# Performance work log

Measured on AMD Instinct MI355X. Metric: run time of the kernel, lower is better.

The kernel has to match this reference:

```python
import jax, jax.numpy as jnp
import numpy as np

LOSS_WEIGHT = 1.0

def setup_inputs() -> dict:
    key = jax.random.key(0)
    k1, k2 = jax.random.split(key)
    B, M, N = 4, 8192, 8192
    pred_colors = jax.random.uniform(k1, (B, M, 3), dtype=jnp.float32)
    gt_colors = jax.random.uniform(k2, (B, N, 3), dtype=jnp.float32)
    return {"pred_colors": pred_colors, "gt_colors": gt_colors}

def reference(pred_colors, gt_colors):
    # torch.cdist(p=2): Euclidean distance matrix [B, M, N]
    # ||a-b||^2 = ||a||^2 + ||b||^2 - 2 a.b
    a2 = jnp.sum(pred_colors * pred_colors, axis=-1)  # [B, M]
    b2 = jnp.sum(gt_colors * gt_colors, axis=-1)      # [B, N]
    ab = jnp.einsum('bmd,bnd->bmn', pred_colors, gt_colors)  # [B, M, N]
    d2 = a2[:, :, None] + b2[:, None, :] - 2.0 * ab
    dists = jnp.sqrt(jnp.maximum(d2, 0.0))
    min_dists = jnp.min(dists, axis=2)  # [B, M]
    return min_dists.mean() * LOSS_WEIGHT
```

## Files before the change

kernel.cpp:

```cpp
#include <hip/hip_runtime.h>
#include <math.h>


constexpr int B    = 4;
constexpr int M    = 8192;
constexpr int N    = 8192;
constexpr int BM   = B * M;
constexpr int TPB  = 256;
constexpr int RPT  = 8;
constexpr int PPB  = TPB * RPT;
constexpr int MBLK = M / PPB;
constexpr int TILE = 1024;

template <int NSEG, bool FINAL>
__global__ __launch_bounds__(TPB)
void k_min(const float* __restrict__ pred, const float* __restrict__ gt,
           float* __restrict__ ws_min, float* __restrict__ out)
{
  constexpr int S  = N / NSEG;
  constexpr int CH = (TILE < NSEG ? TILE : NSEG);
  const int bid = blockIdx.x;
  const int seg = bid % S;
  const int mb  = (bid / S) % MBLK;
  const int b   = bid / (S * MBLK);
  const int t   = threadIdx.x;

  __shared__ float4 tile[CH];

  float cx[RPT], cy[RPT], cz[RPT], mn[RPT];
  const int mbase = mb * PPB + t;
#pragma unroll
  for (int r = 0; r < RPT; ++r) {
    const float* a = pred + ((size_t)b * M + (mbase + r * TPB)) * 3;
    cx[r] = -2.0f * a[0];
    cy[r] = -2.0f * a[1];
    cz[r] = -2.0f * a[2];
    mn[r] = 3.0e38f;
  }

  const int nbase = seg * NSEG;
  for (int n0 = 0; n0 < NSEG; n0 += CH) {
    __syncthreads();
    for (int i = t; i < CH; i += TPB) {
      const float* g = gt + ((size_t)b * N + (nbase + n0 + i)) * 3;
      float gx = g[0], gy = g[1], gz = g[2];
      tile[i] = make_float4(gx, gy, gz, fmaf(gx, gx, fmaf(gy, gy, gz * gz)));
    }
    __syncthreads();
#pragma unroll 2
    for (int n = 0; n < CH; n += 2) {
      const float4 g0 = tile[n];
      const float4 g1 = tile[n + 1];
#pragma unroll
      for (int r = 0; r < RPT; ++r) {
        float s0 = fmaf(cx[r], g0.x, fmaf(cy[r], g0.y, fmaf(cz[r], g0.z, g0.w)));
        float s1 = fmaf(cx[r], g1.x, fmaf(cy[r], g1.y, fmaf(cz[r], g1.z, g1.w)));
        mn[r] = fminf(fminf(s0, s1), mn[r]);
      }
    }
  }

  if (!FINAL) {
    float* dst = ws_min + (size_t)seg * BM + (size_t)b * M + mbase;
#pragma unroll
    for (int r = 0; r < RPT; ++r) dst[r * TPB] = mn[r];
  } else {
    float sum = 0.0f;
#pragma unroll
    for (int r = 0; r < RPT; ++r) {
      const float* a = pred + ((size_t)b * M + (mbase + r * TPB)) * 3;
      float a2 = fmaf(a[0], a[0], fmaf(a[1], a[1], a[2] * a[2]));
      sum += sqrtf(fmaxf(a2 + mn[r], 0.0f)) * (1.0f / BM);
    }
    for (int off = 32; off > 0; off >>= 1) sum += __shfl_down(sum, off, 64);
    __shared__ float wsum[TPB / 64];
    if ((t & 63) == 0) wsum[t >> 6] = sum;
    __syncthreads();
    if (t == 0) {
      float s2 = 0.0f;
#pragma unroll
      for (int w = 0; w < TPB / 64; ++w) s2 += wsum[w];
      atomicAdd(out, s2);
    }
  }
}

template <int S>
__global__ __launch_bounds__(TPB)
void k_combine(const float* __restrict__ pred, const float* __restrict__ ws_min,
               float* __restrict__ out)
{
  const int p = blockIdx.x * TPB + threadIdx.x;
  float v0 = 3.0e38f, v1 = 3.0e38f, v2 = 3.0e38f, v3 = 3.0e38f;
#pragma unroll
  for (int s = 0; s < S; s += 4) {
    v0 = fminf(v0, ws_min[(size_t)(s + 0) * BM + p]);
    v1 = fminf(v1, ws_min[(size_t)(s + 1) * BM + p]);
    v2 = fminf(v2, ws_min[(size_t)(s + 2) * BM + p]);
    v3 = fminf(v3, ws_min[(size_t)(s + 3) * BM + p]);
  }
  float v = fminf(fminf(v0, v1), fminf(v2, v3));
  const float* a = pred + (size_t)p * 3;
  float a2  = fmaf(a[0], a[0], fmaf(a[1], a[1], a[2] * a[2]));
  float sum = sqrtf(fmaxf(a2 + v, 0.0f)) * (1.0f / BM);
  for (int off = 32; off > 0; off >>= 1) sum += __shfl_down(sum, off, 64);
  __shared__ float wsum[TPB / 64];
  if ((threadIdx.x & 63) == 0) wsum[threadIdx.x >> 6] = sum;
  __syncthreads();
  if (threadIdx.x == 0) {
    float s2 = 0.0f;
#pragma unroll
    for (int w = 0; w < TPB / 64; ++w) s2 += wsum[w];
    atomicAdd(out, s2);
  }
}

extern "C" void kernel_launch(void* const* d_in, const int* in_sizes, int n_in,
                              void* d_out, int out_size, void* d_ws, size_t ws_size,
                              hipStream_t stream)
{
  const float* pred = (const float*)d_in[0];
  const float* gt   = (const float*)d_in[1];
  float* out = (float*)d_out;

  hipMemsetAsync(out, 0, sizeof(float), stream);

  int S = 64;
  while (S > 1 && (size_t)S * BM * sizeof(float) > ws_size) S >>= 1;

  if (S >= 4) {
    float* ws_min = (float*)d_ws;
    const dim3 grid(B * MBLK * S), blk(TPB);
    switch (S) {
      case 64:
        k_min<N / 64, false><<<grid, blk, 0, stream>>>(pred, gt, ws_min, nullptr);
        k_combine<64><<<dim3(BM / TPB), blk, 0, stream>>>(pred, ws_min, out);
        break;
      case 32:
        k_min<N / 32, false><<<grid, blk, 0, stream>>>(pred, gt, ws_min, nullptr);
        k_combine<32><<<dim3(BM / TPB), blk, 0, stream>>>(pred, ws_min, out);
        break;
      case 16:
        k_min<N / 16, false><<<grid, blk, 0, stream>>>(pred, gt, ws_min, nullptr);
        k_combine<16><<<dim3(BM / TPB), blk, 0, stream>>>(pred, ws_min, out);
        break;
      case 8:
        k_min<N / 8, false><<<grid, blk, 0, stream>>>(pred, gt, ws_min, nullptr);
        k_combine<8><<<dim3(BM / TPB), blk, 0, stream>>>(pred, ws_min, out);
        break;
      case 4:
        k_min<N / 4, false><<<grid, blk, 0, stream>>>(pred, gt, ws_min, nullptr);
        k_combine<4><<<dim3(BM / TPB), blk, 0, stream>>>(pred, ws_min, out);
        break;
    }
  } else {
    k_min<N, true><<<dim3(B * MBLK), dim3(TPB), 0, stream>>>(pred, gt, nullptr, out);
  }
}
```

Before: 89.27 us.

## Replace brute-force nearest-neighbor search with uniform-grid spatial binning and ring search

Ground-truth points are counting-sorted into a 16^3 uniform grid per batch, and each query point searches expanding rings of cells until the best distance is provably within the ring radius. The aim is to drop the O(M*N) all-pairs distance evaluation. The grid assumes coordinates lie roughly in [0,1] (clamped cells), and work per thread is data-dependent, which brings divergence and scattered global loads. The brute-force path is kept as a fallback when workspace is too small.

```diff
diff --git a/kernel.cpp b/kernel.cpp
--- a/kernel.cpp
+++ b/kernel.cpp
@@ -2,55 +2,152 @@
 #include <math.h>
 
 
-constexpr int B    = 4;
-constexpr int M    = 8192;
-constexpr int N    = 8192;
-constexpr int BM   = B * M;
-constexpr int TPB  = 256;
-constexpr int RPT  = 8;
-constexpr int PPB  = TPB * RPT;
-constexpr int MBLK = M / PPB;
-constexpr int TILE = 1024;
+constexpr int B  = 4;
+constexpr int M  = 8192;
+constexpr int N  = 8192;
+constexpr int BM = B * M;
+constexpr int G  = 16;
+constexpr int NC = G * G * G;
+constexpr float H = 1.0f / G;
 
-template <int NSEG, bool FINAL>
-__global__ __launch_bounds__(TPB)
-void k_min(const float* __restrict__ pred, const float* __restrict__ gt,
-           float* __restrict__ ws_min, float* __restrict__ out)
+__device__ __forceinline__ int cell_of(float x) {
+  int c = (int)(x * (float)G);
+  return c < 0 ? 0 : (c > G - 1 ? G - 1 : c);
+}
+
+__global__ __launch_bounds__(1024)
+void k_bin(const float* __restrict__ gt, float4* __restrict__ sorted,
+           int* __restrict__ cell_start)
 {
-  constexpr int S  = N / NSEG;
-  constexpr int CH = (TILE < NSEG ? TILE : NSEG);
-  const int bid = blockIdx.x;
-  const int seg = bid % S;
-  const int mb  = (bid / S) % MBLK;
-  const int b   = bid / (S * MBLK);
-  const int t   = threadIdx.x;
+  const int b = blockIdx.x, t = threadIdx.x;
+  const int lane = t & 63, wv = t >> 6;
+  __shared__ int cnt[NC];
+  __shared__ int wtot[16];
 
-  __shared__ float4 tile[CH];
+  for (int c = t; c < NC; c += 1024) cnt[c] = 0;
+  __syncthreads();
 
+  float px[8], py[8], pz[8]; int pc[8];
+  const float* g = gt + (size_t)b * N * 3;
+#pragma unroll
+  for (int i = 0; i < 8; ++i) {
+    const int idx = t + i * 1024;
+    px[i] = g[idx * 3 + 0];
+    py[i] = g[idx * 3 + 1];
+    pz[i] = g[idx * 3 + 2];
+    pc[i] = (cell_of(pz[i]) * G + cell_of(py[i])) * G + cell_of(px[i]);
+    atomicAdd(&cnt[pc[i]], 1);
+  }
+  __syncthreads();
+
+  const int i0 = 4 * t;
+  int v0 = cnt[i0], v1 = cnt[i0 + 1], v2 = cnt[i0 + 2], v3 = cnt[i0 + 3];
+  const int own = v0 + v1 + v2 + v3;
+  int s = own;
+  for (int off = 1; off < 64; off <<= 1) {
+    int nb = __shfl_up(s, off, 64);
+    if (lane >= off) s += nb;
+  }
+  if (lane == 63) wtot[wv] = s;
+  __syncthreads();
+  if (t == 0) {
+    int run = 0;
+#pragma unroll
+    for (int w = 0; w < 16; ++w) { int x = wtot[w]; wtot[w] = run; run += x; }
+  }
+  __syncthreads();
+  const int excl = s - own + wtot[wv];
+  cnt[i0]     = excl;
+  cnt[i0 + 1] = excl + v0;
+  cnt[i0 + 2] = excl + v0 + v1;
+  cnt[i0 + 3] = excl + v0 + v1 + v2;
+  __syncthreads();
+
+  int* cs = cell_start + b * (NC + 1);
+  for (int c = t; c < NC; c += 1024) cs[c] = cnt[c];
+  if (t == 0) cs[NC] = N;
+  __syncthreads();
+
+  float4* dst = sorted + (size_t)b * N;
+#pragma unroll
+  for (int i = 0; i < 8; ++i) {
+    const int pos = atomicAdd(&cnt[pc[i]], 1);
+    dst[pos] = make_float4(px[i], py[i], pz[i], 0.0f);
+  }
+}
+
+__global__ __launch_bounds__(64)
+void k_query(const float* __restrict__ pred, const float4* __restrict__ sorted,
+             const int* __restrict__ cell_start, float* __restrict__ out)
+{
+  const int p = blockIdx.x * 64 + threadIdx.x;
+  const int b = p >> 13;
+  const float* a = pred + (size_t)p * 3;
+  const float ax = a[0], ay = a[1], az = a[2];
+  const int qi = cell_of(ax), qj = cell_of(ay), qk = cell_of(az);
+  const float4* pts = sorted + (size_t)b * N;
+  const int* cs = cell_start + b * (NC + 1);
+
+  float best2 = 3.0e38f;
+  auto scan_seg = [&](int cbase, int xs, int xe) {
+    int s = cs[cbase + xs], e = cs[cbase + xe + 1];
+    for (int i = s; i < e; ++i) {
+      const float4 q = pts[i];
+      const float dx = ax - q.x, dy = ay - q.y, dz = az - q.z;
+      best2 = fminf(best2, fmaf(dx, dx, fmaf(dy, dy, dz * dz)));
+    }
+  };
+
+  for (int r = 0;; ++r) {
+    const int z0 = qk - r < 0 ? 0 : qk - r, z1 = qk + r > G - 1 ? G - 1 : qk + r;
+    for (int z = z0; z <= z1; ++z) {
+      const bool zf = (z == qk - r) || (z == qk + r);
+      const int y0 = qj - r < 0 ? 0 : qj - r, y1 = qj + r > G - 1 ? G - 1 : qj + r;
+      for (int y = y0; y <= y1; ++y) {
+        const int cbase = (z * G + y) * G;
+        if (zf || y == qj - r || y == qj + r) {
+          scan_seg(cbase, qi - r < 0 ? 0 : qi - r, qi + r > G - 1 ? G - 1 : qi + r);
+        } else {
+          if (qi - r >= 0)     scan_seg(cbase, qi - r, qi - r);
+          if (qi + r <= G - 1) scan_seg(cbase, qi + r, qi + r);
+        }
+      }
+    }
+    const float rb = (float)r * H;
+    if (best2 <= rb * rb || r == G - 1) break;
+  }
+
+  float val = sqrtf(best2) * (1.0f / BM);
+  for (int off = 32; off; off >>= 1) val += __shfl_down(val, off, 64);
+  if (threadIdx.x == 0) atomicAdd(out, val);
+}
+
+__global__ __launch_bounds__(256)
+void k_brute(const float* __restrict__ pred, const float* __restrict__ gt,
+             float* __restrict__ out)
+{
+  constexpr int TPB = 256, RPT = 8, PPB = TPB * RPT, MBLK = M / PPB;
+  const int mb = blockIdx.x % MBLK, b = blockIdx.x / MBLK, t = threadIdx.x;
+  __shared__ float4 tile[1024];
   float cx[RPT], cy[RPT], cz[RPT], mn[RPT];
   const int mbase = mb * PPB + t;
 #pragma unroll
   for (int r = 0; r < RPT; ++r) {
     const float* a = pred + ((size_t)b * M + (mbase + r * TPB)) * 3;
-    cx[r] = -2.0f * a[0];
-    cy[r] = -2.0f * a[1];
-    cz[r] = -2.0f * a[2];
+    cx[r] = -2.0f * a[0]; cy[r] = -2.0f * a[1]; cz[r] = -2.0f * a[2];
     mn[r] = 3.0e38f;
   }
-
-  const int nbase = seg * NSEG;
-  for (int n0 = 0; n0 < NSEG; n0 += CH) {
+  for (int n0 = 0; n0 < N; n0 += 1024) {
     __syncthreads();
-    for (int i = t; i < CH; i += TPB) {
-      const float* g = gt + ((size_t)b * N + (nbase + n0 + i)) * 3;
-      float gx = g[0], gy = g[1], gz = g[2];
+    for (int i = t; i < 1024; i += TPB) {
+      const float* gp = gt + ((size_t)b * N + (n0 + i)) * 3;
+      float gx = gp[0], gy = gp[1], gz = gp[2];
       tile[i] = make_float4(gx, gy, gz, fmaf(gx, gx, fmaf(gy, gy, gz * gz)));
     }
     __syncthreads();
 #pragma unroll 2
-    for (int n = 0; n < CH; n += 2) {
-      const float4 g0 = tile[n];
-      const float4 g1 = tile[n + 1];
+    for (int n = 0; n < 1024; n += 2) {
+      const float4 g0 = tile[n], g1 = tile[n + 1];
 #pragma unroll
       for (int r = 0; r < RPT; ++r) {
         float s0 = fmaf(cx[r], g0.x, fmaf(cy[r], g0.y, fmaf(cz[r], g0.z, g0.w)));
@@ -59,60 +156,18 @@
       }
     }
   }
-
-  if (!FINAL) {
-    float* dst = ws_min + (size_t)seg * BM + (size_t)b * M + mbase;
+  float sum = 0.0f;
 #pragma unroll
-    for (int r = 0; r < RPT; ++r) dst[r * TPB] = mn[r];
-  } else {
-    float sum = 0.0f;
-#pragma unroll
-    for (int r = 0; r < RPT; ++r) {
-      const float* a = pred + ((size_t)b * M + (mbase + r * TPB)) * 3;
-      float a2 = fmaf(a[0], a[0], fmaf(a[1], a[1], a[2] * a[2]));
-      sum += sqrtf(fmaxf(a2 + mn[r], 0.0f)) * (1.0f / BM);
-    }
-    for (int off = 32; off > 0; off >>= 1) sum += __shfl_down(sum, off, 64);
-    __shared__ float wsum[TPB / 64];
-    if ((t & 63) == 0) wsum[t >> 6] = sum;
-    __syncthreads();
-    if (t == 0) {
-      float s2 = 0.0f;
-#pragma unroll
-      for (int w = 0; w < TPB / 64; ++w) s2 += wsum[w];
-      atomicAdd(out, s2);
-    }
+  for (int r = 0; r < RPT; ++r) {
+    const float* a = pred + ((size_t)b * M + (mbase + r * TPB)) * 3;
+    float a2 = fmaf(a[0], a[0], fmaf(a[1], a[1], a[2] * a[2]));
+    sum += sqrtf(fmaxf(a2 + mn[r], 0.0f)) * (1.0f / BM);
   }
-}
-
-template <int S>
-__global__ __launch_bounds__(TPB)
-void k_combine(const float* __restrict__ pred, const float* __restrict__ ws_min,
-               float* __restrict__ out)
-{
-  const int p = blockIdx.x * TPB + threadIdx.x;
-  float v0 = 3.0e38f, v1 = 3.0e38f, v2 = 3.0e38f, v3 = 3.0e38f;
-#pragma unroll
-  for (int s = 0; s < S; s += 4) {
-    v0 = fminf(v0, ws_min[(size_t)(s + 0) * BM + p]);
-    v1 = fminf(v1, ws_min[(size_t)(s + 1) * BM + p]);
-    v2 = fminf(v2, ws_min[(size_t)(s + 2) * BM + p]);
-    v3 = fminf(v3, ws_min[(size_t)(s + 3) * BM + p]);
-  }
-  float v = fminf(fminf(v0, v1), fminf(v2, v3));
-  const float* a = pred + (size_t)p * 3;
-  float a2  = fmaf(a[0], a[0], fmaf(a[1], a[1], a[2] * a[2]));
-  float sum = sqrtf(fmaxf(a2 + v, 0.0f)) * (1.0f / BM);
-  for (int off = 32; off > 0; off >>= 1) sum += __shfl_down(sum, off, 64);
-  __shared__ float wsum[TPB / 64];
-  if ((threadIdx.x & 63) == 0) wsum[threadIdx.x >> 6] = sum;
+  for (int off = 32; off; off >>= 1) sum += __shfl_down(sum, off, 64);
+  __shared__ float wsum[4];
+  if ((t & 63) == 0) wsum[t >> 6] = sum;
   __syncthreads();
-  if (threadIdx.x == 0) {
-    float s2 = 0.0f;
-#pragma unroll
-    for (int w = 0; w < TPB / 64; ++w) s2 += wsum[w];
-    atomicAdd(out, s2);
-  }
+  if (t == 0) atomicAdd(out, wsum[0] + wsum[1] + wsum[2] + wsum[3]);
 }
 
 extern "C" void kernel_launch(void* const* d_in, const int* in_sizes, int n_in,
@@ -125,35 +180,13 @@
 
   hipMemsetAsync(out, 0, sizeof(float), stream);
 
-  int S = 64;
-  while (S > 1 && (size_t)S * BM * sizeof(float) > ws_size) S >>= 1;
-
-  if (S >= 4) {
-    float* ws_min = (float*)d_ws;
-    const dim3 grid(B * MBLK * S), blk(TPB);
-    switch (S) {
-      case 64:
-        k_min<N / 64, false><<<grid, blk, 0, stream>>>(pred, gt, ws_min, nullptr);
-        k_combine<64><<<dim3(BM / TPB), blk, 0, stream>>>(pred, ws_min, out);
-        break;
-      case 32:
-        k_min<N / 32, false><<<grid, blk, 0, stream>>>(pred, gt, ws_min, nullptr);
-        k_combine<32><<<dim3(BM / TPB), blk, 0, stream>>>(pred, ws_min, out);
-        break;
-      case 16:
-        k_min<N / 16, false><<<grid, blk, 0, stream>>>(pred, gt, ws_min, nullptr);
-        k_combine<16><<<dim3(BM / TPB), blk, 0, stream>>>(pred, ws_min, out);
-        break;
-      case 8:
-        k_min<N / 8, false><<<grid, blk, 0, stream>>>(pred, gt, ws_min, nullptr);
-        k_combine<8><<<dim3(BM / TPB), blk, 0, stream>>>(pred, ws_min, out);
-        break;
-      case 4:
-        k_min<N / 4, false><<<grid, blk, 0, stream>>>(pred, gt, ws_min, nullptr);
-        k_combine<4><<<dim3(BM / TPB), blk, 0, stream>>>(pred, ws_min, out);
-        break;
-    }
+  const size_t need = (size_t)B * N * sizeof(float4) + (size_t)B * (NC + 1) * sizeof(int);
+  if (ws_size >= need) {
+    float4* sorted   = (float4*)d_ws;
+    int* cell_start  = (int*)((char*)d_ws + (size_t)B * N * sizeof(float4));
+    k_bin<<<dim3(B), dim3(1024), 0, stream>>>(gt, sorted, cell_start);
+    k_query<<<dim3(BM / 64), dim3(64), 0, stream>>>(pred, sorted, cell_start, out);
   } else {
-    k_min<N, true><<<dim3(B * MBLK), dim3(TPB), 0, stream>>>(pred, gt, nullptr, out);
+    k_brute<<<dim3(B * (M / 2048)), dim3(256), 0, stream>>>(pred, gt, out);
   }
 }
```

Result: slower. 122.6 us (+37.4%).
